# Kernel tuning notes

Hardware: AMD Instinct MI355X
Metric: run time of the kernel (lower is better)

The kernel has to match this reference:

```python
import jax, jax.numpy as jnp
import numpy as np

N_NODES = 100000
N_EDGES = 2000000
H = 128


def setup_inputs() -> dict:
    key = jax.random.key(0)
    ks = jax.random.split(key, 5)
    z_src = jax.random.normal(ks[0], (N_NODES, H), dtype=jnp.float32)
    z_dst = jax.random.normal(ks[1], (N_NODES, H), dtype=jnp.float32)
    edge_label_index = jax.random.randint(ks[2], (2, N_EDGES), 0, N_NODES, dtype=jnp.int64)
    # Linear(2H, H) and Linear(H, 1) params (stored as [in, out] for x @ W)
    W1 = jax.random.normal(ks[3], (2 * H, H), dtype=jnp.float32) * (1.0 / np.sqrt(2 * H))
    b1 = jnp.zeros((H,), dtype=jnp.float32)
    W2 = jax.random.normal(ks[4], (H, 1), dtype=jnp.float32) * (1.0 / np.sqrt(H))
    b2 = jnp.zeros((1,), dtype=jnp.float32)
    return {"z_src": z_src, "z_dst": z_dst, "edge_label_index": edge_label_index,
            "W1": W1, "b1": b1, "W2": W2, "b2": b2}


def reference(z_src, z_dst, edge_label_index, W1, b1, W2, b2):
    row, col = edge_label_index[0], edge_label_index[1]
    # gather + concat -> [E, 2H]
    z = jnp.concatenate([z_src[row], z_dst[col]], axis=-1)
    h = jax.nn.relu(z @ W1 + b1)          # [E, H]
    out = h @ W2 + b2                     # [E, 1]
    return out.reshape(-1)
```

## Files before the change

### kernel.cpp

```cpp
#include <hip/hip_runtime.h>

#define HDIM 128

typedef __bf16 bf16_t;
typedef bf16_t bf16x8 __attribute__((ext_vector_type(8)));
typedef float  f32x4  __attribute__((ext_vector_type(4)));

__device__ __forceinline__ unsigned short f2bf_rne(float f) {
    unsigned int u = __float_as_uint(f);
    u += 0x7fffu + ((u >> 16) & 1u);
    return (unsigned short)(u >> 16);
}
__device__ __forceinline__ unsigned int pk_bf2(float a, float b) {
    return (unsigned int)f2bf_rne(a) | ((unsigned int)f2bf_rne(b) << 16);
}

__global__ __launch_bounds__(256) void convert_w1(
    const float* __restrict__ W1, unsigned short* __restrict__ Wt)
{
    const int o = blockIdx.x * 256 + threadIdx.x;
    const int g = o >> 14, rem = o & 16383, n = rem >> 7, k = rem & 127;
    Wt[o] = f2bf_rne(W1[g * 16384 + k * 128 + n]);
}

#define ZP 136
__global__ __launch_bounds__(256) void node_gemm_mfma(
    const float* __restrict__ Zs, const float* __restrict__ Zd,
    const unsigned short* __restrict__ Wt, const float* __restrict__ b1,
    unsigned short* __restrict__ Abuf, unsigned short* __restrict__ Bbuf,
    int M, int gb)
{
    __shared__ unsigned short zs[64 * ZP];

    const bool second = (blockIdx.x >= gb);
    const float* __restrict__ Z          = second ? Zd : Zs;
    const unsigned short* __restrict__ W = Wt + (second ? 128 * 128 : 0);
    unsigned short* __restrict__ C       = second ? Bbuf : Abuf;
    const int bx   = second ? (blockIdx.x - gb) : blockIdx.x;
    const int row0 = bx * 64;
    const int t    = threadIdx.x;

    #pragma unroll
    for (int j = 0; j < 8; ++j) {
        const int u   = t + 256 * j;
        const int row = u >> 5;
        const int c4  = u & 31;
        int rg = row0 + row; if (rg >= M) rg = M - 1;
        const float4 v = *reinterpret_cast<const float4*>(Z + (size_t)rg * HDIM + c4 * 4);
        uint2 p; p.x = pk_bf2(v.x, v.y); p.y = pk_bf2(v.z, v.w);
        *reinterpret_cast<uint2*>(zs + row * ZP + c4 * 4) = p;
    }
    __syncthreads();

    const int lane = t & 63;
    const int wave = t >> 6;
    const int m    = lane & 15;
    const int quad = lane >> 4;

    bf16x8 zf[4];
    {
        const unsigned short* zp = zs + (wave * 16 + m) * ZP + quad * 8;
        #pragma unroll
        for (int ks = 0; ks < 4; ++ks)
            zf[ks] = *reinterpret_cast<const bf16x8*>(zp + ks * 32);
    }

    f32x4 acc[8] = {};
    #pragma unroll
    for (int ct = 0; ct < 8; ++ct) {
        const unsigned short* wp = W + (ct * 16 + m) * HDIM + quad * 8;
        #pragma unroll
        for (int ks = 0; ks < 4; ++ks) {
            const bf16x8 wf = *reinterpret_cast<const bf16x8*>(wp + ks * 32);
            acc[ct] = __builtin_amdgcn_mfma_f32_16x16x32_bf16(wf, zf[ks], acc[ct], 0, 0, 0);
        }
    }

    const int grow = row0 + wave * 16 + m;
    if (grow < M) {
        unsigned short* crow = C + (size_t)grow * HDIM;
        #pragma unroll
        for (int ct = 0; ct < 8; ++ct) {
            const int col = ct * 16 + quad * 4;
            float4 bv = make_float4(0.f, 0.f, 0.f, 0.f);
            if (second) bv = *reinterpret_cast<const float4*>(b1 + col);
            uint2 o;
            o.x = pk_bf2(acc[ct][0] + bv.x, acc[ct][1] + bv.y);
            o.y = pk_bf2(acc[ct][2] + bv.z, acc[ct][3] + bv.w);
            *reinterpret_cast<uint2*>(crow + col) = o;
        }
    }
}

__global__ __launch_bounds__(256) void edge_decode_bf16(
    const unsigned short* __restrict__ A, const unsigned short* __restrict__ Bm,
    const int* __restrict__ idx,
    const float* __restrict__ W2, const float* __restrict__ b2,
    float* __restrict__ out, int E)
{
    const int t   = threadIdx.x;
    const int sub = t & 15;
    const int grp = t >> 4;

    float w2r[8];
    #pragma unroll
    for (int i = 0; i < 8; ++i) w2r[i] = W2[sub * 8 + i];
    const float b2s = b2[0];

    const int stride = gridDim.x * 16;
    for (int e = blockIdx.x * 16 + grp; e < E; e += stride) {
        const int r = idx[e];
        const int c = idx[E + e];
        const uint4 av = *reinterpret_cast<const uint4*>(A  + (size_t)r * HDIM + sub * 8);
        const uint4 bv = *reinterpret_cast<const uint4*>(Bm + (size_t)c * HDIM + sub * 8);

        float s = 0.f;
        #pragma unroll
        for (int i = 0; i < 4; ++i) {
            const unsigned int ua = (&av.x)[i];
            const unsigned int ub = (&bv.x)[i];
            s += fmaxf(__uint_as_float(ua << 16)         + __uint_as_float(ub << 16),         0.f) * w2r[2 * i];
            s += fmaxf(__uint_as_float(ua & 0xffff0000u) + __uint_as_float(ub & 0xffff0000u), 0.f) * w2r[2 * i + 1];
        }
        s += __shfl_xor(s, 1);
        s += __shfl_xor(s, 2);
        s += __shfl_xor(s, 4);
        s += __shfl_xor(s, 8);
        if (sub == 0) out[e] = s + b2s;
    }
}

extern "C" void kernel_launch(void* const* d_in, const int* in_sizes, int n_in,
                              void* d_out, int out_size, void* d_ws, size_t ws_size,
                              hipStream_t stream)
{
    const float* z_src = (const float*)d_in[0];
    const float* z_dst = (const float*)d_in[1];
    const int*   eidx  = (const int*)d_in[2];
    const float* W1    = (const float*)d_in[3];
    const float* b1    = (const float*)d_in[4];
    const float* W2    = (const float*)d_in[5];
    const float* b2    = (const float*)d_in[6];
    float*       outp  = (float*)d_out;

    const int Nn = in_sizes[0] / HDIM;
    const int E  = in_sizes[2] / 2;

    unsigned short* Abuf = (unsigned short*)d_ws;
    unsigned short* Bbuf = Abuf + (size_t)Nn * HDIM;
    unsigned short* Wt   = Bbuf + (size_t)Nn * HDIM;

    convert_w1<<<128, 256, 0, stream>>>(W1, Wt);

    const int gb = (Nn + 63) / 64;
    node_gemm_mfma<<<2 * gb, 256, 0, stream>>>(z_src, z_dst, Wt, b1, Abuf, Bbuf, Nn, gb);

    edge_decode_bf16<<<8192, 256, 0, stream>>>(Abuf, Bbuf, eidx, W2, b2, outp, E);
}
```

Measured before the change: 329.6 us.

## Stage W1 tile in LDS and use persistent blocks looping over node tiles

The node GEMM now loads the bf16 W1 half into shared memory once per block and runs a persistent grid of 1024 blocks that loop over 64-row node tiles. Each lane reads its Z row fragments directly from global memory and converts them to bf16 in registers instead of staging Z through LDS. This removes the repeated global W reads per tile and the Z staging barrier, but it lowers the grid size and adds strided global Z loads per lane. The edge decode kernel, which likely dominates the runtime, is unchanged.

```diff
diff --git a/kernel.cpp b/kernel.cpp
--- a/kernel.cpp
+++ b/kernel.cpp
@@ -1,6 +1,8 @@
 #include <hip/hip_runtime.h>
 
 #define HDIM 128
+#define ZP   136
+#define NBH  512
 
 typedef __bf16 bf16_t;
 typedef bf16_t bf16x8 __attribute__((ext_vector_type(8)));
@@ -23,32 +25,27 @@
     Wt[o] = f2bf_rne(W1[g * 16384 + k * 128 + n]);
 }
 
-#define ZP 136
-__global__ __launch_bounds__(256) void node_gemm_mfma(
+__global__ __launch_bounds__(256) void node_gemm_v3(
     const float* __restrict__ Zs, const float* __restrict__ Zd,
     const unsigned short* __restrict__ Wt, const float* __restrict__ b1,
     unsigned short* __restrict__ Abuf, unsigned short* __restrict__ Bbuf,
-    int M, int gb)
+    int M)
 {
-    __shared__ unsigned short zs[64 * ZP];
+    __shared__ unsigned short wlds[128 * ZP];
 
-    const bool second = (blockIdx.x >= gb);
+    const bool second = (blockIdx.x >= NBH);
     const float* __restrict__ Z          = second ? Zd : Zs;
     const unsigned short* __restrict__ W = Wt + (second ? 128 * 128 : 0);
     unsigned short* __restrict__ C       = second ? Bbuf : Abuf;
-    const int bx   = second ? (blockIdx.x - gb) : blockIdx.x;
-    const int row0 = bx * 64;
-    const int t    = threadIdx.x;
+    const int bx = second ? (blockIdx.x - NBH) : blockIdx.x;
+    const int t  = threadIdx.x;
 
     #pragma unroll
     for (int j = 0; j < 8; ++j) {
-        const int u   = t + 256 * j;
-        const int row = u >> 5;
-        const int c4  = u & 31;
-        int rg = row0 + row; if (rg >= M) rg = M - 1;
-        const float4 v = *reinterpret_cast<const float4*>(Z + (size_t)rg * HDIM + c4 * 4);
-        uint2 p; p.x = pk_bf2(v.x, v.y); p.y = pk_bf2(v.z, v.w);
-        *reinterpret_cast<uint2*>(zs + row * ZP + c4 * 4) = p;
+        const int u = t + 256 * j;
+        const int n = u >> 4, c = u & 15;
+        const uint4 v = *reinterpret_cast<const uint4*>(W + n * 128 + c * 8);
+        *reinterpret_cast<uint4*>(wlds + n * ZP + c * 8) = v;
     }
     __syncthreads();
 
@@ -57,37 +54,43 @@
     const int m    = lane & 15;
     const int quad = lane >> 4;
 
-    bf16x8 zf[4];
-    {
-        const unsigned short* zp = zs + (wave * 16 + m) * ZP + quad * 8;
-        #pragma unroll
-        for (int ks = 0; ks < 4; ++ks)
-            zf[ks] = *reinterpret_cast<const bf16x8*>(zp + ks * 32);
-    }
+    const int ntiles = (M + 63) >> 6;
+    for (int tile = bx; tile < ntiles; tile += NBH) {
+        const int row0 = tile * 64;
+        const int r    = row0 + wave * 16 + m;
+        const int rc   = (r < M) ? r : (M - 1);
+        const float* zrow = Z + (size_t)rc * HDIM;
 
-    f32x4 acc[8] = {};
-    #pragma unroll
-    for (int ct = 0; ct < 8; ++ct) {
-        const unsigned short* wp = W + (ct * 16 + m) * HDIM + quad * 8;
+        f32x4 acc[8] = {};
         #pragma unroll
         for (int ks = 0; ks < 4; ++ks) {
-            const bf16x8 wf = *reinterpret_cast<const bf16x8*>(wp + ks * 32);
-            acc[ct] = __builtin_amdgcn_mfma_f32_16x16x32_bf16(wf, zf[ks], acc[ct], 0, 0, 0);
+            const float4 v0 = *reinterpret_cast<const float4*>(zrow + ks * 32 + quad * 8);
+            const float4 v1 = *reinterpret_cast<const float4*>(zrow + ks * 32 + quad * 8 + 4);
+            union { unsigned int u[4]; bf16x8 h; } zf;
+            zf.u[0] = pk_bf2(v0.x, v0.y);
+            zf.u[1] = pk_bf2(v0.z, v0.w);
+            zf.u[2] = pk_bf2(v1.x, v1.y);
+            zf.u[3] = pk_bf2(v1.z, v1.w);
+            #pragma unroll
+            for (int ct = 0; ct < 8; ++ct) {
+                const bf16x8 wf = *reinterpret_cast<const bf16x8*>(
+                    wlds + (ct * 16 + m) * ZP + ks * 32 + quad * 8);
+                acc[ct] = __builtin_amdgcn_mfma_f32_16x16x32_bf16(wf, zf.h, acc[ct], 0, 0, 0);
+            }
         }
-    }
 
-    const int grow = row0 + wave * 16 + m;
-    if (grow < M) {
-        unsigned short* crow = C + (size_t)grow * HDIM;
-        #pragma unroll
-        for (int ct = 0; ct < 8; ++ct) {
-            const int col = ct * 16 + quad * 4;
-            float4 bv = make_float4(0.f, 0.f, 0.f, 0.f);
-            if (second) bv = *reinterpret_cast<const float4*>(b1 + col);
-            uint2 o;
-            o.x = pk_bf2(acc[ct][0] + bv.x, acc[ct][1] + bv.y);
-            o.y = pk_bf2(acc[ct][2] + bv.z, acc[ct][3] + bv.w);
-            *reinterpret_cast<uint2*>(crow + col) = o;
+        if (r < M) {
+            unsigned short* crow = C + (size_t)r * HDIM;
+            #pragma unroll
+            for (int ct = 0; ct < 8; ++ct) {
+                const int col = ct * 16 + quad * 4;
+                float4 bv = make_float4(0.f, 0.f, 0.f, 0.f);
+                if (second) bv = *reinterpret_cast<const float4*>(b1 + col);
+                uint2 o;
+                o.x = pk_bf2(acc[ct][0] + bv.x, acc[ct][1] + bv.y);
+                o.y = pk_bf2(acc[ct][2] + bv.z, acc[ct][3] + bv.w);
+                *reinterpret_cast<uint2*>(crow + col) = o;
+            }
         }
     }
 }
@@ -152,8 +155,7 @@
 
     convert_w1<<<128, 256, 0, stream>>>(W1, Wt);
 
-    const int gb = (Nn + 63) / 64;
-    node_gemm_mfma<<<2 * gb, 256, 0, stream>>>(z_src, z_dst, Wt, b1, Abuf, Bbuf, Nn, gb);
+    node_gemm_v3<<<2 * NBH, 256, 0, stream>>>(z_src, z_dst, Wt, b1, Abuf, Bbuf, Nn);
 
     edge_decode_bf16<<<8192, 256, 0, stream>>>(Abuf, Bbuf, eidx, W2, b2, outp, E);
 }
```

After: 292.2 us. 1.13x faster.
